# Performance work log

Measured on AMD Instinct MI355X. Metric: run time of the kernel, lower is better.

Reference implementation:

```python
import jax, jax.numpy as jnp
import numpy as np

GRID_SIZE = 5
SPLINE_ORDER = 3
KH, KW = 3, 3
STRIDE, PAD, DIL = 1, 1, 1


def make_grid(in_features, dtype=jnp.float32):
    # uniform grid over [-1, 1], extended by spline_order on each side
    h = 2.0 / GRID_SIZE
    g = jnp.arange(-SPLINE_ORDER, GRID_SIZE + SPLINE_ORDER + 1, dtype=dtype) * h - 1.0
    return jnp.broadcast_to(g, (in_features, g.shape[0]))  # (in, G)


def b_splines(x, grid):
    # x: (N, in); grid: (in, G). Cox-de Boor recursion.
    xg = x[..., None]  # (N, in, 1)
    bases = ((xg >= grid[:, :-1]) & (xg < grid[:, 1:])).astype(x.dtype)  # (N, in, G-1)
    for k in range(1, SPLINE_ORDER + 1):
        left = (xg - grid[:, : -(k + 1)]) / (grid[:, k:-1] - grid[:, : -(k + 1)])
        right = (grid[:, k + 1:] - xg) / (grid[:, k + 1:] - grid[:, 1:-k])
        bases = left * bases[..., :-1] + right * bases[..., 1:]
    return bases  # (N, in, grid_size + spline_order)


def setup_inputs() -> dict:
    key = jax.random.key(0)
    k1, k2, k3, k4 = jax.random.split(key, 4)
    B, C, H, W = 4, 64, 64, 64
    out_ch = 128
    patch_dim = C * KH * KW  # 576
    nbasis = GRID_SIZE + SPLINE_ORDER  # 8
    x = jax.random.normal(k1, (B, C, H, W), dtype=jnp.float32)
    base_weight = jax.random.normal(k2, (out_ch, patch_dim), dtype=jnp.float32) * 0.05
    spline_weight = jax.random.normal(k3, (out_ch, patch_dim, nbasis), dtype=jnp.float32) * 0.05
    spline_scaler = jax.random.normal(k4, (out_ch, patch_dim), dtype=jnp.float32) * 0.1 + 1.0
    return {"x": x, "base_weight": base_weight, "spline_weight": spline_weight, "spline_scaler": spline_scaler}


def reference(x, base_weight, spline_weight, spline_scaler):
    B, C, H, W = x.shape
    out_ch, patch_dim = base_weight.shape
    # im2col: (B, C*KH*KW, Ho, Wo), feature dim ordered (C, kh, kw) like F.unfold
    patches = jax.lax.conv_general_dilated_patches(
        x, filter_shape=(KH, KW), window_strides=(STRIDE, STRIDE),
        padding=((PAD, PAD), (PAD, PAD)), rhs_dilation=(DIL, DIL),
        dimension_numbers=("NCHW", "OIHW", "NCHW"))
    Ho = (H + 2 * PAD - DIL * (KH - 1) - 1) // STRIDE + 1
    Wo = (W + 2 * PAD - DIL * (KW - 1) - 1) // STRIDE + 1
    L = Ho * Wo
    p = patches.reshape(B, patch_dim, L).transpose(0, 2, 1).reshape(B * L, patch_dim)  # (N, D)
    grid = make_grid(patch_dim, p.dtype)
    base_out = jax.nn.silu(p) @ base_weight.T  # (N, out)
    bases = b_splines(p, grid)  # (N, D, nbasis)
    scaled_w = spline_weight * spline_scaler[..., None]  # (out, D, nbasis)
    spline_out = jnp.einsum("ndk,odk->no", bases, scaled_w)
    out = (base_out + spline_out).reshape(B, L, out_ch).transpose(0, 2, 1).reshape(B, out_ch, Ho, Wo)
    return out
```

## Files before the change

### kernel.cpp

```cpp
#include <hip/hip_runtime.h>
#include <hip/hip_bf16.h>

#define B_      4
#define C_IN    64
#define H_      64
#define W_      64
#define OUT_CH  128
#define HP_     66
#define CF      576
#define WP_BYTES  (9 * OUT_CH * CF * 2)
#define F_BYTES   (B_ * HP_ * HP_ * CF * 2)
#define P_OFFSET  (WP_BYTES + F_BYTES)

typedef __bf16 bf16x8 __attribute__((ext_vector_type(8)));
typedef float  f32x4  __attribute__((ext_vector_type(4)));
typedef _Float16 half8 __attribute__((ext_vector_type(8)));

__device__ __forceinline__ void compute_features(float x, float f[9]) {
    f[0] = x / (1.0f + __expf(-x));
    float g[12];
#pragma unroll
    for (int i = 0; i < 12; ++i) g[i] = (float)(i - 3) * 0.4f - 1.0f;
    float bb[11];
#pragma unroll
    for (int i = 0; i < 11; ++i) bb[i] = (x >= g[i] && x < g[i + 1]) ? 1.0f : 0.0f;
#pragma unroll
    for (int i = 0; i < 10; ++i)
        bb[i] = (x - g[i]) * (1.0f / (g[i + 1] - g[i])) * bb[i]
              + (g[i + 2] - x) * (1.0f / (g[i + 2] - g[i + 1])) * bb[i + 1];
#pragma unroll
    for (int i = 0; i < 9; ++i)
        bb[i] = (x - g[i]) * (1.0f / (g[i + 2] - g[i])) * bb[i]
              + (g[i + 3] - x) * (1.0f / (g[i + 3] - g[i + 1])) * bb[i + 1];
#pragma unroll
    for (int i = 0; i < 8; ++i)
        bb[i] = (x - g[i]) * (1.0f / (g[i + 3] - g[i])) * bb[i]
              + (g[i + 4] - x) * (1.0f / (g[i + 4] - g[i + 1])) * bb[i + 1];
#pragma unroll
    for (int i = 0; i < 8; ++i) f[1 + i] = bb[i];
}

__global__ __launch_bounds__(256) void pack_kernel(
        const float* __restrict__ bw, const float* __restrict__ sw,
        const float* __restrict__ sc, __hip_bfloat16* __restrict__ Wp) {
    int idx = blockIdx.x * 256 + threadIdx.x;
    if (idx < 589824) {
        int o = idx / 4608;
        int r = idx - o * 4608;
        int d = r >> 3;
        int j = r & 7;
        int tap = d % 9;
        int c   = d / 9;
        float v = sw[idx] * sc[o * 576 + d];
        Wp[(tap * OUT_CH + o) * CF + (j + 1) * 64 + c] = __float2bfloat16(v);
    } else {
        int k = idx - 589824;
        int o = k / 576;
        int d = k - o * 576;
        int tap = d % 9;
        int c   = d / 9;
        Wp[(tap * OUT_CH + o) * CF + c] = __float2bfloat16(bw[k]);
    }
}

__global__ __launch_bounds__(256) void feat_kernel(
        const float* __restrict__ x, __hip_bfloat16* __restrict__ F) {
    __shared__ float xs[64][65];
    int b  = blockIdx.x / HP_;
    int hp = blockIdx.x % HP_;
    int h  = hp - 1;
    int tid = threadIdx.x;

    float f0[9];
    compute_features(0.0f, f0);

    bool interior_row = (h >= 0) && (h < H_);
    if (interior_row) {
        int wl  = tid & 63;
        int c16 = tid >> 6;
#pragma unroll
        for (int i = 0; i < 16; ++i) {
            int c = c16 * 16 + i;
            xs[c][wl] = x[((b * C_IN + c) * H_ + h) * W_ + wl];
        }
    }
    __syncthreads();

    int c  = tid & 63;
    int wg = tid >> 6;
    __hip_bfloat16* Frow = F + (size_t)((b * HP_ + hp) * HP_) * CF;

    if (!interior_row) {
        for (int wp = wg; wp < HP_; wp += 4) {
            __hip_bfloat16* dst = Frow + (size_t)wp * CF + c;
#pragma unroll
            for (int j = 0; j < 9; ++j) dst[j * 64] = __float2bfloat16(f0[j]);
        }
        return;
    }
    if (wg == 0) {
        __hip_bfloat16* dst = Frow + c;
#pragma unroll
        for (int j = 0; j < 9; ++j) dst[j * 64] = __float2bfloat16(f0[j]);
    }
    if (wg == 3) {
        __hip_bfloat16* dst = Frow + (size_t)65 * CF + c;
#pragma unroll
        for (int j = 0; j < 9; ++j) dst[j * 64] = __float2bfloat16(f0[j]);
    }
    for (int w2 = wg; w2 < 64; w2 += 4) {
        float xv = xs[c][w2];
        float f[9];
        compute_features(xv, f);
        __hip_bfloat16* dst = Frow + (size_t)(w2 + 1) * CF + c;
#pragma unroll
        for (int j = 0; j < 9; ++j) dst[j * 64] = __float2bfloat16(f[j]);
    }
}

__global__ __launch_bounds__(256, 2) void gemm_kernel(
        const __hip_bfloat16* __restrict__ Fb, const __hip_bfloat16* __restrict__ Wpb,
        _Float16* __restrict__ P) {
    __shared__ __align__(16) ushort As[2][8192];
    __shared__ __align__(16) ushort Bs[2][8192];

    const ushort* F  = (const ushort*)Fb;
    const ushort* Wp = (const ushort*)Wpb;

    int tid  = threadIdx.x;
    int lane = tid & 63;
    int w    = tid >> 6;
    int l15  = lane & 15;
    int lq   = lane >> 4;
    int wm = w & 1;
    int wn = w >> 1;
    int srow = lane >> 3;
    int sl7  = lane & 7;
    int c8s  = sl7 ^ srow;

    int blk = blockIdx.x;
    int g   = blk >> 7;
    int t   = blk & 127;
    int b   = t >> 5;
    int ho0 = (t & 31) << 1;
    int c0 = (g == 0) ? 0 : (21 + 20 * (g - 1));
    int c1 = c0 + ((g == 0) ? 21 : 20);

    f32x4 acc[4][4];
#pragma unroll
    for (int i = 0; i < 4; ++i)
#pragma unroll
        for (int j = 0; j < 4; ++j) acc[i][j] = (f32x4){0.f, 0.f, 0.f, 0.f};

    auto prefetch = [&](int ch, int buf) {
        int tap = ch / 9;
        int kc  = ch - tap * 9;
        int kh  = tap / 3;
        int kw  = tap - kh * 3;
#pragma unroll
        for (int r = 0; r < 4; ++r) {
            int row = (r * 4 + w) * 8 + srow;
            int hp = ho0 + (row >> 6) + kh;
            int wp = (row & 63) + kw;
            const ushort* srcA = F + (size_t)((b * HP_ + hp) * HP_ + wp) * CF
                                   + kc * 64 + c8s * 8;
            __builtin_amdgcn_global_load_lds(
                (const __attribute__((address_space(1))) unsigned int*)srcA,
                (__attribute__((address_space(3))) unsigned int*)&As[buf][(r * 4 + w) * 512],
                16, 0, 0);
            const ushort* srcB = Wp + (size_t)(tap * OUT_CH + row) * CF
                                    + kc * 64 + c8s * 8;
            __builtin_amdgcn_global_load_lds(
                (const __attribute__((address_space(1))) unsigned int*)srcB,
                (__attribute__((address_space(3))) unsigned int*)&Bs[buf][(r * 4 + w) * 512],
                16, 0, 0);
        }
    };

    int buf = 0;
    prefetch(c0, 0);
    for (int ch = c0; ch < c1; ++ch) {
        __syncthreads();
        if (ch + 1 < c1) prefetch(ch + 1, buf ^ 1);
#pragma unroll
        for (int ks = 0; ks < 2; ++ks) {
            bf16x8 af[4], bq[4];
#pragma unroll
            for (int mt = 0; mt < 4; ++mt) {
                int o  = wm * 64 + mt * 16 + l15;
                int sl = o * 8 + ((ks * 4 + lq) ^ (o & 7));
                af[mt] = *(const bf16x8*)&Bs[buf][sl * 8];
            }
#pragma unroll
            for (int nt = 0; nt < 4; ++nt) {
                int p  = wn * 64 + nt * 16 + l15;
                int sl = p * 8 + ((ks * 4 + lq) ^ (p & 7));
                bq[nt] = *(const bf16x8*)&As[buf][sl * 8];
            }
#pragma unroll
            for (int mt = 0; mt < 4; ++mt)
#pragma unroll
                for (int nt = 0; nt < 4; ++nt)
                    acc[mt][nt] = __builtin_amdgcn_mfma_f32_16x16x32_bf16(
                        af[mt], bq[nt], acc[mt][nt], 0, 0, 0);
        }
        buf ^= 1;
    }

    _Float16* Pg = P + ((size_t)(g * 4 + b) * OUT_CH) * 4096 + ho0 * 64;
#pragma unroll
    for (int mt = 0; mt < 4; ++mt) {
        int o = wm * 64 + mt * 16 + lq * 4;
#pragma unroll
        for (int nt = 0; nt < 4; ++nt) {
            int pix = wn * 64 + nt * 16 + l15;
            _Float16* dst = Pg + (size_t)o * 4096 + pix;
#pragma unroll
            for (int r = 0; r < 4; ++r)
                dst[(size_t)r * 4096] = (_Float16)acc[mt][nt][r];
        }
    }
}

__global__ __launch_bounds__(256) void reduce_kernel(
        const half8* __restrict__ P, float4* __restrict__ out) {
    const int GS = 262144;
    int i = blockIdx.x * 256 + threadIdx.x;
    half8 a = P[i], bb = P[GS + i], c = P[2 * GS + i], d = P[3 * GS + i];
    float4 o0, o1;
#pragma unroll
    for (int j = 0; j < 4; ++j)
        ((float*)&o0)[j] = (float)a[j] + (float)bb[j] + (float)c[j] + (float)d[j];
#pragma unroll
    for (int j = 0; j < 4; ++j)
        ((float*)&o1)[j] = (float)a[4 + j] + (float)bb[4 + j] + (float)c[4 + j] + (float)d[4 + j];
    out[i * 2]     = o0;
    out[i * 2 + 1] = o1;
}

extern "C" void kernel_launch(void* const* d_in, const int* in_sizes, int n_in,
                              void* d_out, int out_size, void* d_ws, size_t ws_size,
                              hipStream_t stream) {
    const float* x  = (const float*)d_in[0];
    const float* bw = (const float*)d_in[1];
    const float* sw = (const float*)d_in[2];
    const float* sc = (const float*)d_in[3];
    float* out = (float*)d_out;

    __hip_bfloat16* Wp = (__hip_bfloat16*)d_ws;
    __hip_bfloat16* F  = (__hip_bfloat16*)((char*)d_ws + WP_BYTES);
    _Float16*       P  = (_Float16*)((char*)d_ws + P_OFFSET);

    pack_kernel<<<2592, 256, 0, stream>>>(bw, sw, sc, Wp);
    feat_kernel<<<B_ * HP_, 256, 0, stream>>>(x, F);
    gemm_kernel<<<512, 256, 0, stream>>>(F, Wp, P);
    reduce_kernel<<<1024, 256, 0, stream>>>((const half8*)P, (float4*)out);
}
```

Measured before the change: 116.2 us.

## Fuse pack and feature kernels; restructure GEMM LDS pipeline with early buffer reuse

Merges the weight-packing and feature kernels into one launch. The feature part now splits each padded row across two blocks, so more blocks run in parallel. The GEMM main loop now issues the next chunk's global loads before the one after that, using explicit vmcnt waits. It loads all LDS fragments into registers first, then refills the freed buffer while the MFMAs run, and raises wave priority around the MFMA burst. The goal is to cut launch overhead and hide global-to-LDS latency behind the matrix math, at the cost of more registers and hand-written waitcnt logic that may be fragile.

```diff
diff --git a/kernel.cpp b/kernel.cpp
--- a/kernel.cpp
+++ b/kernel.cpp
@@ -40,48 +40,53 @@
     for (int i = 0; i < 8; ++i) f[1 + i] = bb[i];
 }
 
-__global__ __launch_bounds__(256) void pack_kernel(
+__global__ __launch_bounds__(256) void prep_kernel(
+        const float* __restrict__ x, __hip_bfloat16* __restrict__ F,
         const float* __restrict__ bw, const float* __restrict__ sw,
         const float* __restrict__ sc, __hip_bfloat16* __restrict__ Wp) {
-    int idx = blockIdx.x * 256 + threadIdx.x;
-    if (idx < 589824) {
-        int o = idx / 4608;
-        int r = idx - o * 4608;
-        int d = r >> 3;
-        int j = r & 7;
-        int tap = d % 9;
-        int c   = d / 9;
-        float v = sw[idx] * sc[o * 576 + d];
-        Wp[(tap * OUT_CH + o) * CF + (j + 1) * 64 + c] = __float2bfloat16(v);
-    } else {
-        int k = idx - 589824;
-        int o = k / 576;
-        int d = k - o * 576;
-        int tap = d % 9;
-        int c   = d / 9;
-        Wp[(tap * OUT_CH + o) * CF + c] = __float2bfloat16(bw[k]);
-    }
-}
-
-__global__ __launch_bounds__(256) void feat_kernel(
-        const float* __restrict__ x, __hip_bfloat16* __restrict__ F) {
-    __shared__ float xs[64][65];
-    int b  = blockIdx.x / HP_;
-    int hp = blockIdx.x % HP_;
+    __shared__ float xs[64][33];
+    int blk = blockIdx.x;
+    int tid = threadIdx.x;
+
+    if (blk >= 528) {
+        int idx = (blk - 528) * 256 + tid;
+        if (idx < 589824) {
+            int o = idx / 4608;
+            int r = idx - o * 4608;
+            int d = r >> 3;
+            int j = r & 7;
+            int tap = d % 9;
+            int c   = d / 9;
+            float v = sw[idx] * sc[o * 576 + d];
+            Wp[(tap * OUT_CH + o) * CF + (j + 1) * 64 + c] = __float2bfloat16(v);
+        } else {
+            int k = idx - 589824;
+            int o = k / 576;
+            int d = k - o * 576;
+            int tap = d % 9;
+            int c   = d / 9;
+            Wp[(tap * OUT_CH + o) * CF + c] = __float2bfloat16(bw[k]);
+        }
+        return;
+    }
+
+    int half = blk & 1;
+    int bh   = blk >> 1;
+    int b  = bh / HP_;
+    int hp = bh % HP_;
     int h  = hp - 1;
-    int tid = threadIdx.x;
 
     float f0[9];
     compute_features(0.0f, f0);
 
     bool interior_row = (h >= 0) && (h < H_);
     if (interior_row) {
-        int wl  = tid & 63;
-        int c16 = tid >> 6;
-#pragma unroll
-        for (int i = 0; i < 16; ++i) {
-            int c = c16 * 16 + i;
-            xs[c][wl] = x[((b * C_IN + c) * H_ + h) * W_ + wl];
+        int wl = tid & 31;
+        int c8 = tid >> 5;
+#pragma unroll
+        for (int i = 0; i < 8; ++i) {
+            int c = c8 * 8 + i;
+            xs[c][wl] = x[((b * C_IN + c) * H_ + h) * W_ + half * 32 + wl];
         }
     }
     __syncthreads();
@@ -91,28 +96,29 @@
     __hip_bfloat16* Frow = F + (size_t)((b * HP_ + hp) * HP_) * CF;
 
     if (!interior_row) {
-        for (int wp = wg; wp < HP_; wp += 4) {
+        for (int wp = half * 33 + wg; wp < half * 33 + 33; wp += 4) {
             __hip_bfloat16* dst = Frow + (size_t)wp * CF + c;
 #pragma unroll
             for (int j = 0; j < 9; ++j) dst[j * 64] = __float2bfloat16(f0[j]);
         }
         return;
     }
-    if (wg == 0) {
+    if (half == 0 && wg == 0) {
         __hip_bfloat16* dst = Frow + c;
 #pragma unroll
         for (int j = 0; j < 9; ++j) dst[j * 64] = __float2bfloat16(f0[j]);
     }
-    if (wg == 3) {
+    if (half == 1 && wg == 3) {
         __hip_bfloat16* dst = Frow + (size_t)65 * CF + c;
 #pragma unroll
         for (int j = 0; j < 9; ++j) dst[j * 64] = __float2bfloat16(f0[j]);
     }
-    for (int w2 = wg; w2 < 64; w2 += 4) {
-        float xv = xs[c][w2];
+    for (int w2l = wg; w2l < 32; w2l += 4) {
+        float xv = xs[c][w2l];
         float f[9];
         compute_features(xv, f);
-        __hip_bfloat16* dst = Frow + (size_t)(w2 + 1) * CF + c;
+        int wp = half * 32 + w2l + 1;
+        __hip_bfloat16* dst = Frow + (size_t)wp * CF + c;
 #pragma unroll
         for (int j = 0; j < 9; ++j) dst[j * 64] = __float2bfloat16(f[j]);
     }
@@ -179,31 +185,40 @@
 
     int buf = 0;
     prefetch(c0, 0);
+    prefetch(c0 + 1, 1);
     for (int ch = c0; ch < c1; ++ch) {
-        __syncthreads();
-        if (ch + 1 < c1) prefetch(ch + 1, buf ^ 1);
+        if (ch + 1 < c1) asm volatile("s_waitcnt vmcnt(8)\n\ts_barrier" ::: "memory");
+        else             asm volatile("s_waitcnt vmcnt(0)\n\ts_barrier" ::: "memory");
+
+        bf16x8 af[2][4], bq[2][4];
 #pragma unroll
         for (int ks = 0; ks < 2; ++ks) {
-            bf16x8 af[4], bq[4];
 #pragma unroll
             for (int mt = 0; mt < 4; ++mt) {
                 int o  = wm * 64 + mt * 16 + l15;
                 int sl = o * 8 + ((ks * 4 + lq) ^ (o & 7));
-                af[mt] = *(const bf16x8*)&Bs[buf][sl * 8];
+                af[ks][mt] = *(const bf16x8*)&Bs[buf][sl * 8];
             }
 #pragma unroll
             for (int nt = 0; nt < 4; ++nt) {
                 int p  = wn * 64 + nt * 16 + l15;
                 int sl = p * 8 + ((ks * 4 + lq) ^ (p & 7));
-                bq[nt] = *(const bf16x8*)&As[buf][sl * 8];
+                bq[ks][nt] = *(const bf16x8*)&As[buf][sl * 8];
             }
+        }
+        asm volatile("s_waitcnt lgkmcnt(0)\n\ts_barrier" ::: "memory");
+        if (ch + 2 < c1) prefetch(ch + 2, buf);
+
+        __builtin_amdgcn_s_setprio(1);
+#pragma unroll
+        for (int ks = 0; ks < 2; ++ks)
 #pragma unroll
             for (int mt = 0; mt < 4; ++mt)
 #pragma unroll
                 for (int nt = 0; nt < 4; ++nt)
                     acc[mt][nt] = __builtin_amdgcn_mfma_f32_16x16x32_bf16(
-                        af[mt], bq[nt], acc[mt][nt], 0, 0, 0);
-        }
+                        af[ks][mt], bq[ks][nt], acc[mt][nt], 0, 0, 0);
+        __builtin_amdgcn_s_setprio(0);
         buf ^= 1;
     }
 
@@ -251,8 +266,7 @@
     __hip_bfloat16* F  = (__hip_bfloat16*)((char*)d_ws + WP_BYTES);
     _Float16*       P  = (_Float16*)((char*)d_ws + P_OFFSET);
 
-    pack_kernel<<<2592, 256, 0, stream>>>(bw, sw, sc, Wp);
-    feat_kernel<<<B_ * HP_, 256, 0, stream>>>(x, F);
+    prep_kernel<<<528 + 2592, 256, 0, stream>>>(x, F, bw, sw, sc, Wp);
     gemm_kernel<<<512, 256, 0, stream>>>(F, Wp, P);
     reduce_kernel<<<1024, 256, 0, stream>>>((const half8*)P, (float4*)out);
 }
```

New measurement: 104.9 us. -9.7%, faster.
